# Performance work log

Measured on AMD Instinct MI355X. Metric: run time of the kernel, lower is better.

The kernel has to match this reference:

```python
import jax, jax.numpy as jnp
import numpy as np

D_MODEL, D_STATE, D_INNER, DT_RANK, D_CONV, K = 768, 16, 1536, 48, 3, 2
B_SZ, L_SEQ = 2, 2048

def setup_inputs() -> dict:
    key = jax.random.key(0)
    ks = jax.random.split(key, 10)
    s = lambda k, shp, sc=0.02: jax.random.normal(k, shp, dtype=jnp.float32) * sc
    return {
        "x": jax.random.normal(ks[0], (B_SZ, L_SEQ, D_MODEL), dtype=jnp.float32),
        "in_proj_w": s(ks[1], (2 * D_INNER, D_MODEL)),
        "conv_w": s(ks[2], (D_INNER, 1, D_CONV), 0.3),
        "conv_b": s(ks[3], (D_INNER,), 0.1),
        "x_proj_w": s(ks[4], (K, DT_RANK + 2 * D_STATE, D_INNER)),
        "dt_proj_w": s(ks[5], (K, D_INNER, DT_RANK), 0.1),
        "dt_proj_b": s(ks[6], (K, D_INNER), 0.1),
        "A_logs": s(ks[7], (K * D_INNER, D_STATE), 0.5),
        "Ds": jnp.ones((K * D_INNER,), dtype=jnp.float32),
        "out_proj_w": s(ks[8], (D_MODEL, D_INNER)),
    }

def _selective_scan(u, delta, A, Bp, Cp, Dk):
    # u, delta: [B, L, D]; A: [D, N]; Bp, Cp: [B, L, N]; Dk: [D]
    def step(h, inp):
        d_t, u_t, b_t, c_t = inp  # [B,D], [B,D], [B,N], [B,N]
        dA = jnp.exp(d_t[..., None] * A)  # [B,D,N]
        h = h * dA + (d_t * u_t)[..., None] * b_t[:, None, :]
        y_t = jnp.einsum('bdn,bn->bd', h, c_t)
        return h, y_t
    h0 = jnp.zeros((u.shape[0], u.shape[2], A.shape[1]), dtype=u.dtype)
    xs = (jnp.swapaxes(delta, 0, 1), jnp.swapaxes(u, 0, 1),
          jnp.swapaxes(Bp, 0, 1), jnp.swapaxes(Cp, 0, 1))
    _, ys = jax.lax.scan(step, h0, xs)  # ys: [L, B, D]
    return jnp.swapaxes(ys, 0, 1) + u * Dk  # [B, L, D]

def _direction(u_k, xw_k, dtw_k, dtb_k, Alog_k, D_k):
    x_dbl = jnp.einsum('bld,rd->blr', u_k, xw_k)
    dt_in, Bp, Cp = jnp.split(x_dbl, [DT_RANK, DT_RANK + D_STATE], axis=-1)
    delta = jax.nn.softplus(jnp.einsum('blr,dr->bld', dt_in, dtw_k) + dtb_k)
    A = -jnp.exp(Alog_k)
    return _selective_scan(u_k, delta, A, Bp, Cp, D_k)

def reference(x, in_proj_w, conv_w, conv_b, x_proj_w, dt_proj_w, dt_proj_b, A_logs, Ds, out_proj_w):
    xz = x @ in_proj_w.T                       # [B, L, 2*Din]
    x_conv, z = jnp.split(xz, 2, axis=-1)
    xc = jnp.swapaxes(x_conv, 1, 2)            # [B, Din, L]
    pad = (D_CONV - 1) // 2
    xc = jax.lax.conv_general_dilated(
        xc, conv_w, window_strides=(1,), padding=[(pad, pad)],
        feature_group_count=D_INNER, dimension_numbers=('NCH', 'OIH', 'NCH'))
    xc = xc + conv_b[None, :, None]
    u = jnp.swapaxes(jax.nn.silu(xc), 1, 2)    # [B, L, Din]

    u_dirs = jnp.stack([u, jnp.flip(u, axis=1)])          # [K, B, L, Din]
    A_logs_k = A_logs.reshape(K, D_INNER, D_STATE)
    Ds_k = Ds.reshape(K, D_INNER)
    y_dirs = jax.vmap(_direction)(u_dirs, x_proj_w, dt_proj_w, dt_proj_b, A_logs_k, Ds_k)
    y_scanned = y_dirs[0] + jnp.flip(y_dirs[1], axis=1)
    y_gated = y_scanned * z
    return y_gated @ out_proj_w.T
```

## Files before the change

kernel.cpp:

```cpp
#include <hip/hip_runtime.h>
#include <math.h>

#define D_MODEL 768
#define D_STATE 16
#define D_INNER 1536
#define DT_RANK 48
#define B_SZ    2
#define L_SEQ   2048
#define CH      32
#define NCH     (L_SEQ / CH)
#define NDG     24
#define MTOT    (B_SZ * L_SEQ)
#define LOG2E   1.4426950408889634f
#define LN2     0.6931471805599453f

typedef __bf16 bf16x8 __attribute__((ext_vector_type(8)));
typedef float f32x4 __attribute__((ext_vector_type(4)));
typedef ushort ushort8_t __attribute__((ext_vector_type(8)));

__device__ __forceinline__ float ex2(float x) {
  return __builtin_amdgcn_exp2f(x);
}

__device__ __forceinline__ ushort f2bf(float f) {
  unsigned int u = __float_as_uint(f);
  unsigned int r = (u + 0x7fff + ((u >> 16) & 1)) >> 16;
  return (ushort)r;
}
__device__ __forceinline__ float bf2f(ushort u) {
  return __uint_as_float(((unsigned int)u) << 16);
}

__device__ __forceinline__ void gload_lds16(const ushort* g, ushort* l) {
  __builtin_amdgcn_global_load_lds(
      (__attribute__((address_space(1))) void*)(void*)(g),
      (__attribute__((address_space(3))) void*)(void*)(l), 16, 0, 0);
}

__device__ __forceinline__ float softplus_fast(float x) {
  return (x > 20.f) ? x : LN2 * __log2f(1.f + ex2(x * LOG2E));
}

template <int BM, int BN, int ACT, int OBF, int DTOUT>
__device__ __forceinline__ void gemm_body(
    const ushort* __restrict__ A, int lda, const ushort* __restrict__ B,
    int ldb, const float* __restrict__ bias, void* __restrict__ Cp, int ldc,
    int Nreal, int K, int bxi, int byi, ushort* __restrict__ dtin,
    float* __restrict__ bcp) {
  __shared__ ushort As[2][BM][32];
  __shared__ ushort Bs[2][BN][32];
  constexpr int WM = BM / 2, WN = BN / 2;
  constexpr int FM = WM / 16, FN = WN / 16;
  const int tid = threadIdx.x;
  const int lane = tid & 63;
  const int w = tid >> 6;
  const int wr = w >> 1, wc = w & 1;
  const int bm = byi * BM, bn = bxi * BN;
  const int lrow = lane >> 2;
  const int lchunk = lane & 3;
  const int fr = lane & 15;
  const int k8 = (lane >> 4) * 8;

  f32x4 acc[FM][FN] = {};

  auto stage = [&](int buf, int k0) {
    if constexpr (BM >= 64) {
#pragma unroll
      for (int g = 0; g < BM / 64; ++g) {
        const int rb = w * (BM / 4) + g * 16;
        gload_lds16(A + (size_t)(bm + rb + lrow) * lda + k0 + lchunk * 8,
                    &As[buf][rb][0]);
      }
    } else {
      if (w < 2)
        gload_lds16(A + (size_t)(bm + w * 16 + lrow) * lda + k0 + lchunk * 8,
                    &As[buf][w * 16][0]);
    }
#pragma unroll
    for (int g = 0; g < BN / 64; ++g) {
      const int rb = w * (BN / 4) + g * 16;
      gload_lds16(B + (size_t)(bn + rb + lrow) * ldb + k0 + lchunk * 8,
                  &Bs[buf][rb][0]);
    }
  };

  stage(0, 0);
  __syncthreads();
  int cur = 0;
  for (int k0 = 0; k0 < K; k0 += 32) {
    if (k0 + 32 < K) stage(cur ^ 1, k0 + 32);
    bf16x8 af[FM], bfr[FN];
#pragma unroll
    for (int m = 0; m < FM; ++m)
      af[m] =
          *reinterpret_cast<const bf16x8*>(&As[cur][wr * WM + m * 16 + fr][k8]);
#pragma unroll
    for (int n = 0; n < FN; ++n)
      bfr[n] =
          *reinterpret_cast<const bf16x8*>(&Bs[cur][wc * WN + n * 16 + fr][k8]);
#pragma unroll
    for (int m = 0; m < FM; ++m)
#pragma unroll
      for (int n = 0; n < FN; ++n)
        acc[m][n] = __builtin_amdgcn_mfma_f32_16x16x32_bf16(af[m], bfr[n],
                                                            acc[m][n], 0, 0, 0);
    __syncthreads();
    cur ^= 1;
  }

  const int row4 = (lane >> 4) * 4;
#pragma unroll
  for (int m = 0; m < FM; ++m) {
#pragma unroll
    for (int n = 0; n < FN; ++n) {
      const int gn = bn + wc * WN + n * 16 + fr;
      const int gm0 = bm + wr * WM + m * 16 + row4;
#pragma unroll
      for (int j = 0; j < 4; ++j) {
        const float v = acc[m][n][j];
        const int gm = gm0 + j;
        if (DTOUT) {
          if (gn < 64)
            dtin[(size_t)gm * 64 + gn] = (gn < 48) ? f2bf(v) : (ushort)0;
          else if (gn >= 80 && gn < 144)
            dtin[(size_t)MTOT * 64 + (size_t)gm * 64 + (gn - 80)] =
                (gn < 128) ? f2bf(v) : (ushort)0;
          if (gn >= 48 && gn < 80)
            bcp[(size_t)gm * 32 + (gn - 48)] = v;
          else if (gn >= 128 && gn < 160)
            bcp[(size_t)MTOT * 32 + (size_t)gm * 32 + (gn - 128)] = v;
        }
        if (gn < Nreal) {
          float vv = v + (bias ? bias[gn] : 0.f);
          if (ACT == 1) vv = softplus_fast(vv);
          if (OBF)
            ((ushort*)Cp)[(size_t)gm * ldc + gn] = f2bf(vv);
          else
            ((float*)Cp)[(size_t)gm * ldc + gn] = vv;
        }
      }
    }
  }
}

template <int BM, int BN, int ACT, int OBF, int DTOUT>
__global__ __launch_bounds__(256) void gemm_k(
    const ushort* __restrict__ A, int lda, const ushort* __restrict__ B,
    int ldb, const float* __restrict__ bias, void* __restrict__ Cp, int ldc,
    int Nreal, int K, ushort* __restrict__ dtin, float* __restrict__ bcp) {
  gemm_body<BM, BN, ACT, OBF, DTOUT>(A, lda, B, ldb, bias, Cp, ldc, Nreal, K,
                                     blockIdx.x, blockIdx.y, dtin, bcp);
}

__global__ __launch_bounds__(256) void gemm_dt_k(
    const ushort* __restrict__ dtin, const ushort* __restrict__ w_dt,
    const float* __restrict__ dtb, ushort* __restrict__ delta) {
  const int k = blockIdx.z;
  gemm_body<64, 128, 1, 1, 0>(
      dtin + (size_t)k * MTOT * 64, 64, w_dt + (size_t)k * D_INNER * 64, 64,
      dtb + k * D_INNER, delta + (size_t)k * MTOT * D_INNER, D_INNER, D_INNER,
      64, blockIdx.x, blockIdx.y, nullptr, nullptr);
}

__global__ __launch_bounds__(256) void cvt_all_kernel(
    const float* __restrict__ x, const float* __restrict__ w_in,
    const float* __restrict__ w_out, const float* __restrict__ w_xp,
    const float* __restrict__ w_dt, ushort* __restrict__ x_bf,
    ushort* __restrict__ w_in_bf, ushort* __restrict__ w_out_bf,
    ushort* __restrict__ w_xp_bf, ushort* __restrict__ w_dt_bf) {
  const long N0 = 3145728, N1 = 2359296, N2 = 1179648, N3 = 393216, N4 = 196608;
  long i = ((long)blockIdx.x * 256 + threadIdx.x) * 4;
  if (i < N0) {
    const float4 v = *(const float4*)(x + i);
    ushort4 o = {f2bf(v.x), f2bf(v.y), f2bf(v.z), f2bf(v.w)};
    *(ushort4*)(x_bf + i) = o;
    return;
  }
  i -= N0;
  if (i < N1) {
    const float4 v = *(const float4*)(w_in + i);
    ushort4 o = {f2bf(v.x), f2bf(v.y), f2bf(v.z), f2bf(v.w)};
    *(ushort4*)(w_in_bf + i) = o;
    return;
  }
  i -= N1;
  if (i < N2) {
    const float4 v = *(const float4*)(w_out + i);
    ushort4 o = {f2bf(v.x), f2bf(v.y), f2bf(v.z), f2bf(v.w)};
    *(ushort4*)(w_out_bf + i) = o;
    return;
  }
  i -= N2;
  if (i < N3) {
    const long row = i / 1536;
    ushort4 o = {0, 0, 0, 0};
    if (row < 160) {
      const float4 v = *(const float4*)(w_xp + i);
      o.x = f2bf(v.x); o.y = f2bf(v.y); o.z = f2bf(v.z); o.w = f2bf(v.w);
    }
    *(ushort4*)(w_xp_bf + i) = o;
    return;
  }
  i -= N3;
  if (i < N4) {
    const int col = (int)(i & 63);
    const long row = i >> 6;
    ushort4 o = {0, 0, 0, 0};
    if (col < 48) {
      const float4 v = *(const float4*)(w_dt + row * 48 + col);
      o.x = f2bf(v.x); o.y = f2bf(v.y); o.z = f2bf(v.z); o.w = f2bf(v.w);
    }
    *(ushort4*)(w_dt_bf + i) = o;
  }
}

__global__ __launch_bounds__(256) void conv_silu_kernel(
    const ushort* __restrict__ xz, const float* __restrict__ cw,
    const float* __restrict__ cb, ushort* __restrict__ u_bf) {
  const int nd8 = D_INNER / 8;
  const int idx = blockIdx.x * 256 + threadIdx.x;
  const int d8 = idx % nd8;
  const int lg = (idx / nd8) % (L_SEQ / 8);
  const int b = idx / (nd8 * (L_SEQ / 8));
  const int d = d8 * 8;
  const int l0 = lg * 8;

  float w0[8], w1[8], w2[8], bs[8];
#pragma unroll
  for (int j = 0; j < 8; ++j) {
    w0[j] = cw[(d + j) * 3 + 0];
    w1[j] = cw[(d + j) * 3 + 1];
    w2[j] = cw[(d + j) * 3 + 2];
    bs[j] = cb[d + j];
  }
  const ushort* base = xz + ((size_t)b * L_SEQ) * 3072 + d;
  const ushort8_t zv = {0, 0, 0, 0, 0, 0, 0, 0};
  ushort8_t prev = (l0 > 0) ? *(const ushort8_t*)(base + (size_t)(l0 - 1) * 3072) : zv;
  ushort8_t curv = *(const ushort8_t*)(base + (size_t)l0 * 3072);
#pragma unroll
  for (int i = 0; i < 8; ++i) {
    const int l = l0 + i;
    const ushort8_t nxt =
        (l + 1 < L_SEQ) ? *(const ushort8_t*)(base + (size_t)(l + 1) * 3072) : zv;
    ushort8_t o;
#pragma unroll
    for (int j = 0; j < 8; ++j) {
      const float a = bs[j] + bf2f(prev[j]) * w0[j] + bf2f(curv[j]) * w1[j] +
                      bf2f(nxt[j]) * w2[j];
      o[j] = f2bf(a / (1.f + __expf(-a)));
    }
    *(ushort8_t*)(u_bf + ((size_t)b * L_SEQ + l) * D_INNER + d) = o;
    prev = curv;
    curv = nxt;
  }
}

__global__ __launch_bounds__(256) void scan_local_kernel(
    const ushort* __restrict__ u_bf, const float* __restrict__ bcf,
    const ushort* __restrict__ delta_bf, const float* __restrict__ A_logs,
    const float* __restrict__ Ds, ushort* __restrict__ y,
    float* __restrict__ hfin, float* __restrict__ Tsum) {
  __shared__ ushort sD[CH][256];
  __shared__ ushort sU[CH][256];
  __shared__ float sBC[CH][32];
  const int tid = threadIdx.x;
  const int w = tid >> 6;
  const int l = tid & 63;
  const int bid = blockIdx.x;
  const int ch = bid & (NCH - 1);
  const int rest = bid >> 6;
  const int dgB6 = rest % 6;
  const int kb = rest / 6;
  const int b = kb & 1;
  const int k = kb >> 1;
  const int d0 = dgB6 * 256;
  const int d = d0 + tid;
  const int row = k * D_INNER + d;

  float An[16];
#pragma unroll
  for (int q = 0; q < 4; ++q) {
    const float4 a = *(const float4*)(A_logs + (size_t)row * D_STATE + q * 4);
    An[q * 4 + 0] = -__expf(a.x) * LOG2E;
    An[q * 4 + 1] = -__expf(a.y) * LOG2E;
    An[q * 4 + 2] = -__expf(a.z) * LOG2E;
    An[q * 4 + 3] = -__expf(a.w) * LOG2E;
  }
  const float Dk = Ds[row];

  const int t0 = ch * CH;
  const int lbase = k ? (L_SEQ - CH - t0) : t0;
  const ushort* dptr = delta_bf + (size_t)(k * B_SZ + b) * L_SEQ * D_INNER;
  const ushort* uptr = u_bf + (size_t)b * L_SEQ * D_INNER;
  const float* bck = bcf + ((size_t)k * MTOT + (size_t)b * L_SEQ) * 32;
  ushort* yptr = y + (size_t)(k * B_SZ + b) * L_SEQ * D_INNER;

  {
    const int rr = w * 2 + (l >> 5);
    const int seg = l & 31;
#pragma unroll
    for (int i = 0; i < 4; ++i) {
      const int r2 = i * 8 + rr;
      const int gr = k ? (CH - 1 - r2) : r2;
      const size_t off = (size_t)(lbase + gr) * D_INNER + d0 + seg * 8;
      gload_lds16(dptr + off, &sD[0][0] + i * 2048 + w * 512);
      gload_lds16(uptr + off, &sU[0][0] + i * 2048 + w * 512);
    }
  }
  {
    const int r2 = w * 8 + (l >> 3);
    const int gr = k ? (CH - 1 - r2) : r2;
    gload_lds16(
        (const ushort*)(bck + (size_t)(lbase + gr) * 32 + (l & 7) * 4),
        (ushort*)(&sBC[0][0] + w * 256));
  }
  __syncthreads();

  float h[16] = {};
  float S = 0.f;

  for (int s = 0; s < CH; ++s) {
    const float dlt = bf2f(sD[s][tid]);
    const float uu = bf2f(sU[s][tid]);
    S += dlt;
    const float du = dlt * uu;
    const float4 B0 = *(const float4*)&sBC[s][0];
    const float4 B1 = *(const float4*)&sBC[s][4];
    const float4 B2 = *(const float4*)&sBC[s][8];
    const float4 B3 = *(const float4*)&sBC[s][12];
    const float4 C0 = *(const float4*)&sBC[s][16];
    const float4 C1 = *(const float4*)&sBC[s][20];
    const float4 C2 = *(const float4*)&sBC[s][24];
    const float4 C3 = *(const float4*)&sBC[s][28];
    float yt = 0.f;
    h[0] = h[0] * ex2(dlt * An[0]) + du * B0.x;   yt += h[0] * C0.x;
    h[1] = h[1] * ex2(dlt * An[1]) + du * B0.y;   yt += h[1] * C0.y;
    h[2] = h[2] * ex2(dlt * An[2]) + du * B0.z;   yt += h[2] * C0.z;
    h[3] = h[3] * ex2(dlt * An[3]) + du * B0.w;   yt += h[3] * C0.w;
    h[4] = h[4] * ex2(dlt * An[4]) + du * B1.x;   yt += h[4] * C1.x;
    h[5] = h[5] * ex2(dlt * An[5]) + du * B1.y;   yt += h[5] * C1.y;
    h[6] = h[6] * ex2(dlt * An[6]) + du * B1.z;   yt += h[6] * C1.z;
    h[7] = h[7] * ex2(dlt * An[7]) + du * B1.w;   yt += h[7] * C1.w;
    h[8] = h[8] * ex2(dlt * An[8]) + du * B2.x;   yt += h[8] * C2.x;
    h[9] = h[9] * ex2(dlt * An[9]) + du * B2.y;   yt += h[9] * C2.y;
    h[10] = h[10] * ex2(dlt * An[10]) + du * B2.z; yt += h[10] * C2.z;
    h[11] = h[11] * ex2(dlt * An[11]) + du * B2.w; yt += h[11] * C2.w;
    h[12] = h[12] * ex2(dlt * An[12]) + du * B3.x; yt += h[12] * C3.x;
    h[13] = h[13] * ex2(dlt * An[13]) + du * B3.y; yt += h[13] * C3.y;
    h[14] = h[14] * ex2(dlt * An[14]) + du * B3.z; yt += h[14] * C3.z;
    h[15] = h[15] * ex2(dlt * An[15]) + du * B3.w; yt += h[15] * C3.w;
    const int t = t0 + s;
    const int ll = k ? (L_SEQ - 1 - t) : t;
    yptr[(size_t)ll * D_INNER + d] = f2bf(yt + uu * Dk);
  }

  const int dg64 = dgB6 * 4 + w;
  const size_t cidxB = ((size_t)(k * B_SZ + b) * NCH + ch) * NDG + dg64;
#pragma unroll
  for (int q = 0; q < 4; ++q)
    *(float4*)(hfin + cidxB * 1024 + l * 16 + q * 4) =
        make_float4(h[q * 4], h[q * 4 + 1], h[q * 4 + 2], h[q * 4 + 3]);
  Tsum[cidxB * 64 + l] = S;
}

__global__ __launch_bounds__(256) void scan_stitch_kernel(
    const float* __restrict__ hfin, const float* __restrict__ Tsum,
    const float* __restrict__ A_logs, float* __restrict__ hin) {
  const int tid = threadIdx.x;
  const int dl = tid >> 2;
  const int nq = tid & 3;
  const int bid = blockIdx.x;
  const int dgB = bid % NDG;
  const int b = (bid / NDG) & 1;
  const int k = bid / (NDG * 2);
  const int row = k * D_INNER + dgB * 64 + dl;
  const float4 alv = *(const float4*)(A_logs + (size_t)row * D_STATE + nq * 4);
  const float An0 = -__expf(alv.x) * LOG2E, An1 = -__expf(alv.y) * LOG2E;
  const float An2 = -__expf(alv.z) * LOG2E, An3 = -__expf(alv.w) * LOG2E;
  float c0 = 0.f, c1 = 0.f, c2 = 0.f, c3 = 0.f;
  for (int ch = 0; ch < NCH; ++ch) {
    const size_t cidxB = ((size_t)(k * B_SZ + b) * NCH + ch) * NDG + dgB;
    const size_t off = cidxB * 1024 + dl * 16 + nq * 4;
    *(float4*)(hin + off) = make_float4(c0, c1, c2, c3);
    const float T = Tsum[cidxB * 64 + dl];
    const float4 hf = *(const float4*)(hfin + off);
    c0 = c0 * ex2(An0 * T) + hf.x;
    c1 = c1 * ex2(An1 * T) + hf.y;
    c2 = c2 * ex2(An2 * T) + hf.z;
    c3 = c3 * ex2(An3 * T) + hf.w;
  }
}

__global__ __launch_bounds__(256) void fixup_gate_kernel(
    const float* __restrict__ bcf, const ushort* __restrict__ delta_bf,
    const float* __restrict__ A_logs, const float* __restrict__ hin,
    const ushort* __restrict__ y, const ushort* __restrict__ xz_bf,
    ushort* __restrict__ yg) {
  __shared__ ushort sd0[64][64], sd1[64][64];
  __shared__ float sC0f[64][16], sC1f[64][16];
  __shared__ float sQF[64][4], sQB[64][4];
  const int tid = threadIdx.x;
  const int wid = tid >> 6;
  const int lane = tid & 63;
  const int tq = wid;
  const int dl = lane;
  const int bid = blockIdx.x;
  const int chf = bid & 31;
  const int rest = bid >> 5;
  const int dgB = rest % NDG;
  const int b = rest / NDG;
  const int d0 = dgB * 64;
  const int d = d0 + dl;
  const int lbase = chf * 64;

  float AnF[16], AnB[16], hF[16], hB[16];
#pragma unroll
  for (int q = 0; q < 4; ++q) {
    const float4 af = *(const float4*)(A_logs + (size_t)d * D_STATE + q * 4);
    AnF[q * 4 + 0] = -__expf(af.x) * LOG2E;
    AnF[q * 4 + 1] = -__expf(af.y) * LOG2E;
    AnF[q * 4 + 2] = -__expf(af.z) * LOG2E;
    AnF[q * 4 + 3] = -__expf(af.w) * LOG2E;
    const float4 ab =
        *(const float4*)(A_logs + (size_t)(D_INNER + d) * D_STATE + q * 4);
    AnB[q * 4 + 0] = -__expf(ab.x) * LOG2E;
    AnB[q * 4 + 1] = -__expf(ab.y) * LOG2E;
    AnB[q * 4 + 2] = -__expf(ab.z) * LOG2E;
    AnB[q * 4 + 3] = -__expf(ab.w) * LOG2E;
  }
  const int chF = chf * 2 + (tq >> 1);
  const int chB = NCH - 1 - chf * 2 - (tq >> 1);
  const size_t cF = ((size_t)(0 * B_SZ + b) * NCH + chF) * NDG + dgB;
  const size_t cB = ((size_t)(1 * B_SZ + b) * NCH + chB) * NDG + dgB;
#pragma unroll
  for (int q = 0; q < 4; ++q) {
    const float4 hv = *(const float4*)(hin + cF * 1024 + dl * 16 + q * 4);
    hF[q * 4 + 0] = hv.x; hF[q * 4 + 1] = hv.y;
    hF[q * 4 + 2] = hv.z; hF[q * 4 + 3] = hv.w;
    const float4 hw = *(const float4*)(hin + cB * 1024 + dl * 16 + q * 4);
    hB[q * 4 + 0] = hw.x; hB[q * 4 + 1] = hw.y;
    hB[q * 4 + 2] = hw.z; hB[q * 4 + 3] = hw.w;
  }

  const ushort* d0p =
      delta_bf + ((size_t)(0 * B_SZ + b) * L_SEQ + lbase) * D_INNER + d0;
  const ushort* d1p =
      delta_bf + ((size_t)(1 * B_SZ + b) * L_SEQ + lbase) * D_INNER + d0;
  {
    const int rd = lane >> 3, seg = lane & 7;
#pragma unroll
    for (int i = 0; i < 2; ++i) {
      const int sl = i * 4 + wid;
      const int r = sl * 8 + rd;
      const size_t off = (size_t)r * D_INNER + seg * 8;
      gload_lds16(d0p + off, &sd0[0][0] + sl * 512);
      gload_lds16(d1p + off, &sd1[0][0] + sl * 512);
    }
  }
  {
    const float* bc0 = bcf + (size_t)b * L_SEQ * 32;
    const float* bc1 = bcf + (size_t)MTOT * 32 + (size_t)b * L_SEQ * 32;
    const int r = tid >> 2;
    const int q = tid & 3;
    *(float4*)&sC0f[r][q * 4] =
        *(const float4*)(bc0 + (size_t)(lbase + r) * 32 + 16 + q * 4);
    *(float4*)&sC1f[r][q * 4] =
        *(const float4*)(bc1 + (size_t)(lbase + r) * 32 + 16 + q * 4);
  }
  __syncthreads();
  float qf = 0.f, qb = 0.f;
#pragma unroll
  for (int i = 0; i < 16; ++i) {
    qf += bf2f(sd0[tq * 16 + i][dl]);
    qb += bf2f(sd1[tq * 16 + i][dl]);
  }
  sQF[dl][tq] = qf;
  sQB[dl][tq] = qb;
  __syncthreads();
  float SF = (tq & 1) ? sQF[dl][tq - 1] : 0.f;
  float SB = (tq & 1) ? 0.f : sQB[dl][tq + 1];

  const ushort* y0p = y + ((size_t)(0 * B_SZ + b) * L_SEQ) * D_INNER;
  const ushort* y1p = y + ((size_t)(1 * B_SZ + b) * L_SEQ) * D_INNER;
  float yacc[16];
#pragma unroll
  for (int i = 0; i < 16; ++i) {
    const int t = tq * 16 + i;
    SF += bf2f(sd0[t][dl]);
    const float4 C0 = *(const float4*)&sC0f[t][0];
    const float4 C1 = *(const float4*)&sC0f[t][4];
    const float4 C2 = *(const float4*)&sC0f[t][8];
    const float4 C3 = *(const float4*)&sC0f[t][12];
    float wf;
    wf  = C0.x * (ex2(AnF[0] * SF) * hF[0]);
    wf += C0.y * (ex2(AnF[1] * SF) * hF[1]);
    wf += C0.z * (ex2(AnF[2] * SF) * hF[2]);
    wf += C0.w * (ex2(AnF[3] * SF) * hF[3]);
    wf += C1.x * (ex2(AnF[4] * SF) * hF[4]);
    wf += C1.y * (ex2(AnF[5] * SF) * hF[5]);
    wf += C1.z * (ex2(AnF[6] * SF) * hF[6]);
    wf += C1.w * (ex2(AnF[7] * SF) * hF[7]);
    wf += C2.x * (ex2(AnF[8] * SF) * hF[8]);
    wf += C2.y * (ex2(AnF[9] * SF) * hF[9]);
    wf += C2.z * (ex2(AnF[10] * SF) * hF[10]);
    wf += C2.w * (ex2(AnF[11] * SF) * hF[11]);
    wf += C3.x * (ex2(AnF[12] * SF) * hF[12]);
    wf += C3.y * (ex2(AnF[13] * SF) * hF[13]);
    wf += C3.z * (ex2(AnF[14] * SF) * hF[14]);
    wf += C3.w * (ex2(AnF[15] * SF) * hF[15]);
    yacc[i] = bf2f(y0p[(size_t)(lbase + t) * D_INNER + d]) + wf;
  }
#pragma unroll
  for (int i = 15; i >= 0; --i) {
    const int t = tq * 16 + i;
    SB += bf2f(sd1[t][dl]);
    const float4 C0 = *(const float4*)&sC1f[t][0];
    const float4 C1 = *(const float4*)&sC1f[t][4];
    const float4 C2 = *(const float4*)&sC1f[t][8];
    const float4 C3 = *(const float4*)&sC1f[t][12];
    float wb;
    wb  = C0.x * (ex2(AnB[0] * SB) * hB[0]);
    wb += C0.y * (ex2(AnB[1] * SB) * hB[1]);
    wb += C0.z * (ex2(AnB[2] * SB) * hB[2]);
    wb += C0.w * (ex2(AnB[3] * SB) * hB[3]);
    wb += C1.x * (ex2(AnB[4] * SB) * hB[4]);
    wb += C1.y * (ex2(AnB[5] * SB) * hB[5]);
    wb += C1.z * (ex2(AnB[6] * SB) * hB[6]);
    wb += C1.w * (ex2(AnB[7] * SB) * hB[7]);
    wb += C2.x * (ex2(AnB[8] * SB) * hB[8]);
    wb += C2.y * (ex2(AnB[9] * SB) * hB[9]);
    wb += C2.z * (ex2(AnB[10] * SB) * hB[10]);
    wb += C2.w * (ex2(AnB[11] * SB) * hB[11]);
    wb += C3.x * (ex2(AnB[12] * SB) * hB[12]);
    wb += C3.y * (ex2(AnB[13] * SB) * hB[13]);
    wb += C3.z * (ex2(AnB[14] * SB) * hB[14]);
    wb += C3.w * (ex2(AnB[15] * SB) * hB[15]);
    yacc[i] += bf2f(y1p[(size_t)(lbase + t) * D_INNER + d]) + wb;
  }
#pragma unroll
  for (int i = 0; i < 16; ++i) {
    const int l = lbase + tq * 16 + i;
    const float z = bf2f(xz_bf[((size_t)b * L_SEQ + l) * 3072 + 1536 + d]);
    yg[((size_t)b * L_SEQ + l) * D_INNER + d] = f2bf(yacc[i] * z);
  }
}

extern "C" void kernel_launch(void* const* d_in, const int* in_sizes, int n_in,
                              void* d_out, int out_size, void* d_ws,
                              size_t ws_size, hipStream_t stream) {
  const float* x          = (const float*)d_in[0];
  const float* in_proj_w  = (const float*)d_in[1];
  const float* conv_w     = (const float*)d_in[2];
  const float* conv_b     = (const float*)d_in[3];
  const float* x_proj_w   = (const float*)d_in[4];
  const float* dt_proj_w  = (const float*)d_in[5];
  const float* dt_proj_b  = (const float*)d_in[6];
  const float* A_logs     = (const float*)d_in[7];
  const float* Ds         = (const float*)d_in[8];
  const float* out_proj_w = (const float*)d_in[9];
  float* out = (float*)d_out;

  const int M = MTOT;
  const size_t NST = (size_t)2 * B_SZ * NCH * NDG;

  float* ws    = (float*)d_ws;
  float* hfin  = ws;
  float* hin   = hfin + NST * 1024;
  float* Tsum  = hin + NST * 1024;
  float* bcf   = Tsum + NST * 64;
  ushort* x_bf     = (ushort*)(bcf + (size_t)2 * M * 32);
  ushort* w_in_bf  = x_bf + (size_t)M * 768;
  ushort* w_out_bf = w_in_bf + (size_t)3072 * 768;
  ushort* w_xp_bf  = w_out_bf + (size_t)768 * 1536;
  ushort* w_dt_bf  = w_xp_bf + (size_t)256 * 1536;
  ushort* xz_bf    = w_dt_bf + (size_t)2 * 1536 * 64;
  ushort* u_bf     = xz_bf + (size_t)M * 3072;
  ushort* delta_bf = u_bf + (size_t)M * 1536;
  ushort* dtin     = delta_bf + (size_t)2 * M * 1536;
  ushort* y_bf     = dtin + (size_t)2 * M * 64;
  ushort* yg_bf    = y_bf + (size_t)2 * M * 1536;

  dim3 blk(256);

  {
    const long TOT = 3145728L + 2359296 + 1179648 + 393216 + 196608;
    cvt_all_kernel<<<dim3((TOT / 4 + 255) / 256), blk, 0, stream>>>(
        x, in_proj_w, out_proj_w, x_proj_w, dt_proj_w, x_bf, w_in_bf, w_out_bf,
        w_xp_bf, w_dt_bf);
  }

  gemm_k<128, 128, 0, 1, 0><<<dim3(3072 / 128, M / 128), blk, 0, stream>>>(
      x_bf, 768, w_in_bf, 768, nullptr, xz_bf, 3072, 3072, 768, nullptr,
      nullptr);

  conv_silu_kernel<<<dim3(B_SZ * (L_SEQ / 8) * (D_INNER / 8) / 256), blk, 0,
                     stream>>>(xz_bf, conv_w, conv_b, u_bf);

  gemm_k<32, 64, 0, 0, 1><<<dim3(3, M / 32), blk, 0, stream>>>(
      u_bf, 1536, w_xp_bf, 1536, nullptr, nullptr, 1, 0, 1536, dtin, bcf);

  gemm_dt_k<<<dim3(1536 / 128, M / 64, 2), blk, 0, stream>>>(
      dtin, w_dt_bf, dt_proj_b, delta_bf);

  scan_local_kernel<<<dim3(2 * B_SZ * 6 * NCH), blk, 0, stream>>>(
      u_bf, bcf, delta_bf, A_logs, Ds, y_bf, hfin, Tsum);
  scan_stitch_kernel<<<dim3(2 * B_SZ * NDG), blk, 0, stream>>>(hfin, Tsum,
                                                               A_logs, hin);
  fixup_gate_kernel<<<dim3(B_SZ * NDG * (L_SEQ / 64)), blk, 0, stream>>>(
      bcf, delta_bf, A_logs, hin, y_bf, xz_bf, yg_bf);

  gemm_k<128, 128, 0, 0, 0><<<dim3(768 / 128, M / 128), blk, 0, stream>>>(
      yg_bf, 1536, w_out_bf, 1536, nullptr, out, 768, 768, 1536, nullptr,
      nullptr);
}
```

Before: 228.0 us.

## Double scan chunk length to 64 and align fixup blocks with chunks

```diff
diff --git a/kernel.cpp b/kernel.cpp
--- a/kernel.cpp
+++ b/kernel.cpp
@@ -7,7 +7,7 @@
 #define DT_RANK 48
 #define B_SZ    2
 #define L_SEQ   2048
-#define CH      32
+#define CH      64
 #define NCH     (L_SEQ / CH)
 #define NDG     24
 #define MTOT    (B_SZ * L_SEQ)
@@ -260,15 +260,15 @@
     const ushort* __restrict__ delta_bf, const float* __restrict__ A_logs,
     const float* __restrict__ Ds, ushort* __restrict__ y,
     float* __restrict__ hfin, float* __restrict__ Tsum) {
-  __shared__ ushort sD[CH][256];
-  __shared__ ushort sU[CH][256];
+  __shared__ ushort sD[32][256];
+  __shared__ ushort sU[32][256];
   __shared__ float sBC[CH][32];
   const int tid = threadIdx.x;
   const int w = tid >> 6;
   const int l = tid & 63;
   const int bid = blockIdx.x;
   const int ch = bid & (NCH - 1);
-  const int rest = bid >> 6;
+  const int rest = bid >> 5;
   const int dgB6 = rest % 6;
   const int kb = rest / 6;
   const int b = kb & 1;
@@ -296,62 +296,69 @@
   ushort* yptr = y + (size_t)(k * B_SZ + b) * L_SEQ * D_INNER;
 
   {
-    const int rr = w * 2 + (l >> 5);
-    const int seg = l & 31;
-#pragma unroll
-    for (int i = 0; i < 4; ++i) {
-      const int r2 = i * 8 + rr;
+#pragma unroll
+    for (int i = 0; i < 2; ++i) {
+      const int r2 = i * 32 + w * 8 + (l >> 3);
       const int gr = k ? (CH - 1 - r2) : r2;
-      const size_t off = (size_t)(lbase + gr) * D_INNER + d0 + seg * 8;
-      gload_lds16(dptr + off, &sD[0][0] + i * 2048 + w * 512);
-      gload_lds16(uptr + off, &sU[0][0] + i * 2048 + w * 512);
-    }
-  }
-  {
-    const int r2 = w * 8 + (l >> 3);
-    const int gr = k ? (CH - 1 - r2) : r2;
-    gload_lds16(
-        (const ushort*)(bck + (size_t)(lbase + gr) * 32 + (l & 7) * 4),
-        (ushort*)(&sBC[0][0] + w * 256));
-  }
-  __syncthreads();
+      gload_lds16(
+          (const ushort*)(bck + (size_t)(lbase + gr) * 32 + (l & 7) * 4),
+          (ushort*)(&sBC[0][0] + i * 1024 + w * 256));
+    }
+  }
 
   float h[16] = {};
   float S = 0.f;
 
-  for (int s = 0; s < CH; ++s) {
-    const float dlt = bf2f(sD[s][tid]);
-    const float uu = bf2f(sU[s][tid]);
-    S += dlt;
-    const float du = dlt * uu;
-    const float4 B0 = *(const float4*)&sBC[s][0];
-    const float4 B1 = *(const float4*)&sBC[s][4];
-    const float4 B2 = *(const float4*)&sBC[s][8];
-    const float4 B3 = *(const float4*)&sBC[s][12];
-    const float4 C0 = *(const float4*)&sBC[s][16];
-    const float4 C1 = *(const float4*)&sBC[s][20];
-    const float4 C2 = *(const float4*)&sBC[s][24];
-    const float4 C3 = *(const float4*)&sBC[s][28];
-    float yt = 0.f;
-    h[0] = h[0] * ex2(dlt * An[0]) + du * B0.x;   yt += h[0] * C0.x;
-    h[1] = h[1] * ex2(dlt * An[1]) + du * B0.y;   yt += h[1] * C0.y;
-    h[2] = h[2] * ex2(dlt * An[2]) + du * B0.z;   yt += h[2] * C0.z;
-    h[3] = h[3] * ex2(dlt * An[3]) + du * B0.w;   yt += h[3] * C0.w;
-    h[4] = h[4] * ex2(dlt * An[4]) + du * B1.x;   yt += h[4] * C1.x;
-    h[5] = h[5] * ex2(dlt * An[5]) + du * B1.y;   yt += h[5] * C1.y;
-    h[6] = h[6] * ex2(dlt * An[6]) + du * B1.z;   yt += h[6] * C1.z;
-    h[7] = h[7] * ex2(dlt * An[7]) + du * B1.w;   yt += h[7] * C1.w;
-    h[8] = h[8] * ex2(dlt * An[8]) + du * B2.x;   yt += h[8] * C2.x;
-    h[9] = h[9] * ex2(dlt * An[9]) + du * B2.y;   yt += h[9] * C2.y;
-    h[10] = h[10] * ex2(dlt * An[10]) + du * B2.z; yt += h[10] * C2.z;
-    h[11] = h[11] * ex2(dlt * An[11]) + du * B2.w; yt += h[11] * C2.w;
-    h[12] = h[12] * ex2(dlt * An[12]) + du * B3.x; yt += h[12] * C3.x;
-    h[13] = h[13] * ex2(dlt * An[13]) + du * B3.y; yt += h[13] * C3.y;
-    h[14] = h[14] * ex2(dlt * An[14]) + du * B3.z; yt += h[14] * C3.z;
-    h[15] = h[15] * ex2(dlt * An[15]) + du * B3.w; yt += h[15] * C3.w;
-    const int t = t0 + s;
-    const int ll = k ? (L_SEQ - 1 - t) : t;
-    yptr[(size_t)ll * D_INNER + d] = f2bf(yt + uu * Dk);
+  for (int half = 0; half < 2; ++half) {
+    {
+      const int rr = w * 2 + (l >> 5);
+      const int seg = l & 31;
+#pragma unroll
+      for (int i = 0; i < 4; ++i) {
+        const int r2 = i * 8 + rr;
+        const int gr = k ? (CH - 1 - (half * 32 + r2)) : (half * 32 + r2);
+        const size_t off = (size_t)(lbase + gr) * D_INNER + d0 + seg * 8;
+        gload_lds16(dptr + off, &sD[0][0] + i * 2048 + w * 512);
+        gload_lds16(uptr + off, &sU[0][0] + i * 2048 + w * 512);
+      }
+    }
+    __syncthreads();
+    for (int s = 0; s < 32; ++s) {
+      const float dlt = bf2f(sD[s][tid]);
+      const float uu = bf2f(sU[s][tid]);
+      S += dlt;
+      const float du = dlt * uu;
+      const int sb = half * 32 + s;
+      const float4 B0 = *(const float4*)&sBC[sb][0];
+      const float4 B1 = *(const float4*)&sBC[sb][4];
+      const float4 B2 = *(const float4*)&sBC[sb][8];
+      const float4 B3 = *(const float4*)&sBC[sb][12];
+      const float4 C0 = *(const float4*)&sBC[sb][16];
+      const float4 C1 = *(const float4*)&sBC[sb][20];
+      const float4 C2 = *(const float4*)&sBC[sb][24];
+      const float4 C3 = *(const float4*)&sBC[sb][28];
+      float yt = 0.f;
+      h[0] = h[0] * ex2(dlt * An[0]) + du * B0.x;   yt += h[0] * C0.x;
+      h[1] = h[1] * ex2(dlt * An[1]) + du * B0.y;   yt += h[1] * C0.y;
+      h[2] = h[2] * ex2(dlt * An[2]) + du * B0.z;   yt += h[2] * C0.z;
+      h[3] = h[3] * ex2(dlt * An[3]) + du * B0.w;   yt += h[3] * C0.w;
+      h[4] = h[4] * ex2(dlt * An[4]) + du * B1.x;   yt += h[4] * C1.x;
+      h[5] = h[5] * ex2(dlt * An[5]) + du * B1.y;   yt += h[5] * C1.y;
+      h[6] = h[6] * ex2(dlt * An[6]) + du * B1.z;   yt += h[6] * C1.z;
+      h[7] = h[7] * ex2(dlt * An[7]) + du * B1.w;   yt += h[7] * C1.w;
+      h[8] = h[8] * ex2(dlt * An[8]) + du * B2.x;   yt += h[8] * C2.x;
+      h[9] = h[9] * ex2(dlt * An[9]) + du * B2.y;   yt += h[9] * C2.y;
+      h[10] = h[10] * ex2(dlt * An[10]) + du * B2.z; yt += h[10] * C2.z;
+      h[11] = h[11] * ex2(dlt * An[11]) + du * B2.w; yt += h[11] * C2.w;
+      h[12] = h[12] * ex2(dlt * An[12]) + du * B3.x; yt += h[12] * C3.x;
+      h[13] = h[13] * ex2(dlt * An[13]) + du * B3.y; yt += h[13] * C3.y;
+      h[14] = h[14] * ex2(dlt * An[14]) + du * B3.z; yt += h[14] * C3.z;
+      h[15] = h[15] * ex2(dlt * An[15]) + du * B3.w; yt += h[15] * C3.w;
+      const int t = t0 + half * 32 + s;
+      const int ll = k ? (L_SEQ - 1 - t) : t;
+      yptr[(size_t)ll * D_INNER + d] = f2bf(yt + uu * Dk);
+    }
+    __syncthreads();
   }
 
   const int dg64 = dgB6 * 4 + w;
@@ -405,13 +412,14 @@
   const int tq = wid;
   const int dl = lane;
   const int bid = blockIdx.x;
-  const int chf = bid & 31;
+  const int ch = bid & (NCH - 1);
   const int rest = bid >> 5;
   const int dgB = rest % NDG;
   const int b = rest / NDG;
   const int d0 = dgB * 64;
   const int d = d0 + dl;
-  const int lbase = chf * 64;
+  const int lbase = ch * CH;
+  const int chb = NCH - 1 - ch;
 
   float AnF[16], AnB[16], hF[16], hB[16];
 #pragma unroll
@@ -428,10 +436,8 @@
     AnB[q * 4 + 2] = -__expf(ab.z) * LOG2E;
     AnB[q * 4 + 3] = -__expf(ab.w) * LOG2E;
   }
-  const int chF = chf * 2 + (tq >> 1);
-  const int chB = NCH - 1 - chf * 2 - (tq >> 1);
-  const size_t cF = ((size_t)(0 * B_SZ + b) * NCH + chF) * NDG + dgB;
-  const size_t cB = ((size_t)(1 * B_SZ + b) * NCH + chB) * NDG + dgB;
+  const size_t cF = ((size_t)(0 * B_SZ + b) * NCH + ch) * NDG + dgB;
+  const size_t cB = ((size_t)(1 * B_SZ + b) * NCH + chb) * NDG + dgB;
 #pragma unroll
   for (int q = 0; q < 4; ++q) {
     const float4 hv = *(const float4*)(hin + cF * 1024 + dl * 16 + q * 4);
@@ -477,8 +483,12 @@
   sQF[dl][tq] = qf;
   sQB[dl][tq] = qb;
   __syncthreads();
-  float SF = (tq & 1) ? sQF[dl][tq - 1] : 0.f;
-  float SB = (tq & 1) ? 0.f : sQB[dl][tq + 1];
+  float SF = 0.f, SB = 0.f;
+#pragma unroll
+  for (int j = 0; j < 4; ++j) {
+    if (j < tq) SF += sQF[dl][j];
+    if (j > tq) SB += sQB[dl][j];
+  }
 
   const ushort* y0p = y + ((size_t)(0 * B_SZ + b) * L_SEQ) * D_INNER;
   const ushort* y1p = y + ((size_t)(1 * B_SZ + b) * L_SEQ) * D_INNER;
@@ -606,7 +616,7 @@
       u_bf, bcf, delta_bf, A_logs, Ds, y_bf, hfin, Tsum);
   scan_stitch_kernel<<<dim3(2 * B_SZ * NDG), blk, 0, stream>>>(hfin, Tsum,
                                                                A_logs, hin);
-  fixup_gate_kernel<<<dim3(B_SZ * NDG * (L_SEQ / 64)), blk, 0, stream>>>(
+  fixup_gate_kernel<<<dim3(B_SZ * NDG * NCH), blk, 0, stream>>>(
       bcf, delta_bf, A_logs, hin, y_bf, xz_bf, yg_bf);
 
   gemm_k<128, 128, 0, 0, 0><<<dim3(768 / 128, M / 128), blk, 0, stream>>>(
```

Measured after the change: 224.6 us. No clear change (-1.5%).
